# Performance work log

Measured on AMD Instinct MI355X. Metric: run time of the kernel, lower is better.

## Reference

```python
import jax, jax.numpy as jnp
import numpy as np

B, N, F, H1, H2, NC = 1024, 64, 1024, 256, 128, 128
ALPHA = 0.2   # LeakyReLU slope
BN_EPS = 1e-5


def setup_inputs() -> dict:
    key = jax.random.key(0)
    ks = jax.random.split(key, 20)
    d = {}
    d["x"] = jax.random.normal(ks[0], (B, 1, F), dtype=jnp.float32)
    d["neighbor"] = jax.random.normal(ks[1], (B, N, 1, F), dtype=jnp.float32)
    # GraphAttn layer 1 params
    d["W1"] = jax.random.normal(ks[2], (H1, F), dtype=jnp.float32) / np.sqrt(F)
    d["b1"] = jnp.zeros((H1,), dtype=jnp.float32)
    d["a11"] = jax.random.normal(ks[3], (H1,), dtype=jnp.float32) / np.sqrt(H1)
    d["a12"] = jax.random.normal(ks[4], (H1,), dtype=jnp.float32) / np.sqrt(H1)
    d["g1"] = jnp.ones((), dtype=jnp.float32)   # BatchNorm1d(1) weight (scalar)
    d["be1"] = jnp.zeros((), dtype=jnp.float32)  # BatchNorm1d(1) bias
    # GraphAttn layer 2 params
    d["W2"] = jax.random.normal(ks[5], (H2, H1), dtype=jnp.float32) / np.sqrt(H1)
    d["b2"] = jnp.zeros((H2,), dtype=jnp.float32)
    d["a21"] = jax.random.normal(ks[6], (H2,), dtype=jnp.float32) / np.sqrt(H2)
    d["a22"] = jax.random.normal(ks[7], (H2,), dtype=jnp.float32) / np.sqrt(H2)
    d["g2"] = jnp.ones((), dtype=jnp.float32)
    d["be2"] = jnp.zeros((), dtype=jnp.float32)
    # final classifier
    d["Wl"] = jax.random.normal(ks[8], (NC, H2), dtype=jnp.float32) / np.sqrt(H2)
    d["bl"] = jnp.zeros((NC,), dtype=jnp.float32)
    return d


def _l2norm_c(t):
    # torch nf.normalize default: p=2, dim=1 -> here the singleton channel axis (-2)
    n = jnp.sqrt(jnp.sum(t * t, axis=-2, keepdims=True))
    return t / jnp.maximum(n, 1e-12)


def _gat_layer(x, nb, W, b, a_self, a_nb):
    # x: [B,1,Fin], nb: [B,N,1,Fin]
    xh = jnp.einsum('bcf,hf->bch', x, W) + b        # [B,1,H]
    nbh = jnp.einsum('bncf,hf->bnch', nb, W) + b    # [B,N,1,H]
    # att1(x[i]) + att2(neighbor[i]) -> scores over N (C==1 squeezed)
    s = (jnp.einsum('bch,h->bc', xh, a_self)[:, None, :]
         + jnp.einsum('bnch,h->bnc', nbh, a_nb))[..., 0]   # [B,N]
    A = jax.nn.softmax(jax.nn.leaky_relu(s, ALPHA), axis=1)  # softmax over neighbors
    out = jnp.einsum('bn,bnch->bch', A, nbh)        # [B,1,H]
    return out, nbh


def _bn_relu(t, g, b, axes):
    # BatchNorm1d(1) in training mode: stats over all non-channel dims of the tensor
    m = jnp.mean(t, axis=axes, keepdims=True)
    v = jnp.mean(jnp.square(t - m), axis=axes, keepdims=True)
    return jax.nn.relu(g * (t - m) * jax.lax.rsqrt(v + BN_EPS) + b)


def reference(x, neighbor, W1, b1, a11, a12, g1, be1,
              W2, b2, a21, a22, g2, be2, Wl, bl):
    x = _l2norm_c(x)
    nb = _l2norm_c(neighbor)
    x, nb = _gat_layer(x, nb, W1, b1, a11, a12)
    # acvt1 applied to x [B,1,H1] (stats over B,H) and to each neighbor tensor
    # [N,1,H1] separately (per-sample stats -> axes (1,3) of [B,N,1,H1])
    x = _bn_relu(x, g1, be1, axes=(0, 2))
    nb = _bn_relu(nb, g1, be1, axes=(1, 3))
    x, nb = _gat_layer(x, nb, W2, b2, a21, a22)
    x = _bn_relu(x, g2, be2, axes=(0, 2))
    # Flatten -> Dropout(p=0) -> Linear
    logits = jnp.einsum('bh,ch->bc', x.reshape(x.shape[0], -1), Wl) + bl
    return logits
```

## Files before the change

### kernel.cpp

```cpp
#include <hip/hip_runtime.h>
#include <hip/hip_bf16.h>
#include <stdint.h>

#define B_    1024
#define N_    64
#define F_    1024
#define H1_   256
#define H2_   128
#define NC_   128
#define ALPHA 0.2f
#define BN_EPS 1e-5f

typedef __attribute__((ext_vector_type(4))) float  f32x4;
typedef __attribute__((ext_vector_type(8))) __bf16 bf16x8;
typedef __attribute__((ext_vector_type(4))) __bf16 bf16x4;

__device__ inline float sign_ref(float v) {
    float s = copysignf(1.0f, v);
    return (fabsf(v) >= 1e-12f) ? s : v * 1e12f;
}

__device__ __forceinline__ void gload_lds16(const void* g, void* l) {
    auto gp = reinterpret_cast<const __attribute__((address_space(1))) void*>(
        reinterpret_cast<uintptr_t>(g));
    auto lp = reinterpret_cast<__attribute__((address_space(3))) void*>(
        reinterpret_cast<uintptr_t>(l));
    __builtin_amdgcn_global_load_lds(gp, lp, 16, 0, 0);
}

__device__ inline float blk_reduce(float v, float* buf) {
    #pragma unroll
    for (int o = 32; o > 0; o >>= 1) v += __shfl_xor(v, o, 64);
    __syncthreads();
    const int wave = threadIdx.x >> 6, lane = threadIdx.x & 63;
    if (lane == 0) buf[wave] = v;
    __syncthreads();
    float r = 0.f;
    if (threadIdx.x == 0) {
        const int nw = blockDim.x >> 6;
        for (int i = 0; i < nw; ++i) r += buf[i];
    }
    return r;
}

__global__ __launch_bounds__(256) void k_prep(
    const float* __restrict__ W1, const float* __restrict__ W2,
    const float* __restrict__ b1, const float* __restrict__ a11,
    const float* __restrict__ a12, const float* __restrict__ b2,
    const float* __restrict__ a21, const float* __restrict__ a22,
    __bf16* __restrict__ W1b, __bf16* __restrict__ W2b,
    float* __restrict__ w1a, float* __restrict__ w2a,
    float* __restrict__ w2a22, float* __restrict__ cscal)
{
    __shared__ float rbuf[8];
    const int blk = blockIdx.x, tid = threadIdx.x;
    if (blk < 256) {
        const int i0 = blk * 1024 + tid * 4;
        float4 v = *(const float4*)(W1 + i0);
        bf16x4 p = { (__bf16)v.x, (__bf16)v.y, (__bf16)v.z, (__bf16)v.w };
        *(bf16x4*)(W1b + i0) = p;
    } else if (blk < 288) {
        const int i0 = (blk - 256) * 1024 + tid * 4;
        float4 v = *(const float4*)(W2 + i0);
        bf16x4 p = { (__bf16)v.x, (__bf16)v.y, (__bf16)v.z, (__bf16)v.w };
        *(bf16x4*)(W2b + i0) = p;
    } else if (blk < 292) {
        const int f = (blk - 288) * 256 + tid;
        float s1 = 0.f;
        for (int h = 0; h < H1_; ++h) s1 += W1[h * F_ + f] * a11[h];
        w1a[f] = s1;
    } else if (blk == 292) {
        float s1 = 0.f, s2 = 0.f;
        for (int h = 0; h < H2_; ++h) {
            const float w = W2[h * H1_ + tid];
            s1 += w * a21[h]; s2 += w * a22[h];
        }
        w2a[tid] = s1; w2a22[tid] = s2;
    } else {
        float v1 = b1[tid] * a11[tid];
        float v2 = (tid < H2_) ? b2[tid] * a21[tid] : 0.f;
        float v3 = (tid < H2_) ? b2[tid] * a22[tid] : 0.f;
        float r1 = blk_reduce(v1, rbuf);
        float r2 = blk_reduce(v2, rbuf);
        float r3 = blk_reduce(v3, rbuf);
        if (tid == 0) { cscal[0] = r1; cscal[1] = r2; cscal[2] = r3; }
    }
}

__global__ __launch_bounds__(256, 1) void k_gemm1(
    const float* __restrict__ A, const __bf16* __restrict__ Bw,
    const float* __restrict__ bias, __bf16* __restrict__ C)
{
    constexpr int BM = 128, BN = 256, BK = 64, K = F_;
    constexpr int LDA = BK + 8;
    __shared__ __attribute__((aligned(16))) char smem[BM * LDA * 2 + BN * BK * 2];
    __bf16* As = (__bf16*)smem;
    __bf16* Bs = (__bf16*)(smem + BM * LDA * 2);
    __bf16* Cs = Bs;

    const int tid = threadIdx.x;
    const int wave = tid >> 6, lane = tid & 63;
    const int wm = wave & 1, wn = wave >> 1;
    const int rowin = lane & 15, kq = lane >> 4;
    const size_t m0 = (size_t)blockIdx.x * BM;

    f32x4 acc[4][8] = {};

    const int cqA = tid & 15, r0A = tid >> 4;
    const float* Abase = A + m0 * K + cqA * 4;

    for (int k0 = 0; k0 < K; k0 += BK) {
        #pragma unroll
        for (int it = 0; it < 8; ++it) {
            const int s = it * 256 + tid;
            const int r = s >> 3;
            const int c8 = (s & 7) ^ (r & 7);
            gload_lds16(Bw + (size_t)r * K + k0 + c8 * 8, Bs + s * 8);
        }
        #pragma unroll
        for (int rr = 0; rr < 8; ++rr) {
            const int r = r0A + rr * 16;
            float4 v = *(const float4*)(Abase + (size_t)r * K + k0);
            bf16x4 p = { (__bf16)sign_ref(v.x), (__bf16)sign_ref(v.y),
                         (__bf16)sign_ref(v.z), (__bf16)sign_ref(v.w) };
            *(bf16x4*)&As[r * LDA + cqA * 4] = p;
        }
        __syncthreads();
        #pragma unroll
        for (int ks = 0; ks < 2; ++ks) {
            bf16x8 af[4], bv[8];
            #pragma unroll
            for (int mi = 0; mi < 4; ++mi)
                af[mi] = *(const bf16x8*)&As[(wm * 64 + mi * 16 + rowin) * LDA + ks * 32 + kq * 8];
            #pragma unroll
            for (int ni = 0; ni < 8; ++ni) {
                const int r = wn * 128 + ni * 16 + rowin;
                const int c = (ks * 4 + kq) ^ (r & 7);
                bv[ni] = *(const bf16x8*)&Bs[(r * 8 + c) * 8];
            }
            #pragma unroll
            for (int mi = 0; mi < 4; ++mi)
                #pragma unroll
                for (int ni = 0; ni < 8; ++ni)
                    acc[mi][ni] = __builtin_amdgcn_mfma_f32_16x16x32_bf16(
                        af[mi], bv[ni], acc[mi][ni], 0, 0, 0);
        }
        __syncthreads();
    }
    const int cr0 = (lane >> 4) * 4, cc = lane & 15;
    for (int half = 0; half < 2; ++half) {
        if (wm == half) {
            #pragma unroll
            for (int ni = 0; ni < 8; ++ni) {
                const int col = wn * 128 + ni * 16 + cc;
                const float bs = bias[col];
                #pragma unroll
                for (int mi = 0; mi < 4; ++mi)
                    #pragma unroll
                    for (int i = 0; i < 4; ++i)
                        Cs[(mi * 16 + cr0 + i) * 256 + col] =
                            (__bf16)(acc[mi][ni][i] + bs);
            }
        }
        __syncthreads();
        #pragma unroll
        for (int it = 0; it < 8; ++it) {
            const int s = it * 256 + tid;
            const size_t row = m0 + half * 64 + (s >> 5);
            *(bf16x8*)(C + row * 256 + (s & 31) * 8) = *(const bf16x8*)&Cs[s * 8];
        }
        __syncthreads();
    }
}

__global__ __launch_bounds__(256) void k_front(
    const float* __restrict__ x, const float* __restrict__ w1a,
    const __bf16* __restrict__ nbh1, const float* __restrict__ a12,
    const float* __restrict__ g1p, const float* __restrict__ be1p,
    const float* __restrict__ cscal,
    float* __restrict__ out1, float* __restrict__ alpha1,
    float* __restrict__ beta1, float* __restrict__ psum1,
    float* __restrict__ psq1)
{
    __shared__ __attribute__((aligned(16))) __bf16 tile[N_ * H1_];
    __shared__ float a12s[H1_];
    __shared__ float sv[N_];
    __shared__ float rbuf[8];
    __shared__ float sscal[1];

    const int b = blockIdx.x, tid = threadIdx.x;

    const float* xb = x + (size_t)b * F_;
    float xv[4], wa[4];
    #pragma unroll
    for (int i = 0; i < 4; ++i) { xv[i] = xb[tid + i * 256]; wa[i] = w1a[tid + i * 256]; }
    const __bf16* src = nbh1 + (size_t)b * N_ * H1_;
    #pragma unroll
    for (int it = 0; it < 8; ++it)
        gload_lds16(src + (it * 256 + tid) * 8, tile + (it * 256 + tid) * 8);
    a12s[tid] = a12[tid];
    float p0 = 0.f;
    #pragma unroll
    for (int i = 0; i < 4; ++i) p0 += sign_ref(xv[i]) * wa[i];
    float r0 = blk_reduce(p0, rbuf);
    if (tid == 0) sscal[0] = r0 + cscal[0];
    __syncthreads();

    {
        const int n = tid >> 2, q = tid & 3;
        float p = 0.f;
        for (int i = 0; i < 64; ++i) {
            const int h = q * 64 + ((i + tid) & 63);
            p += (float)tile[n * H1_ + h] * a12s[h];
        }
        p += __shfl_xor(p, 1); p += __shfl_xor(p, 2);
        if (q == 0) { float s = sscal[0] + p; sv[n] = s > 0.f ? s : ALPHA * s; }
    }
    __syncthreads();
    if (tid < 64) {
        float s = sv[tid], m = s;
        #pragma unroll
        for (int o = 1; o < 64; o <<= 1) m = fmaxf(m, __shfl_xor(m, o));
        float e = __expf(s - m), t = e;
        #pragma unroll
        for (int o = 1; o < 64; o <<= 1) t += __shfl_xor(t, o);
        sv[tid] = e / t;
    }
    __syncthreads();

    float o1 = 0.f, ss = 0.f, sq = 0.f;
    for (int n2 = 0; n2 < N_; ++n2) {
        const float v = (float)tile[n2 * H1_ + tid];
        o1 += sv[n2] * v; ss += v; sq += v * v;
    }
    out1[(size_t)b * H1_ + tid] = o1;
    {
        const float rs = blk_reduce(ss, rbuf);
        const float rq = blk_reduce(sq, rbuf);
        if (tid == 0) {
            const float inv = 1.f / (float)(N_ * H1_);
            const float mean = rs * inv, var = rq * inv - mean * mean;
            const float a = (*g1p) * rsqrtf(var + BN_EPS);
            alpha1[b] = a; beta1[b] = (*be1p) - a * mean;
        }
        const float rsx = blk_reduce(o1, rbuf);
        const float rqx = blk_reduce(o1 * o1, rbuf);
        if (tid == 0) { psum1[b] = rsx; psq1[b] = rqx; }
    }
}

__global__ __launch_bounds__(256) void k_back(
    const __bf16* __restrict__ nbh1, const float* __restrict__ out1,
    const float* __restrict__ alpha1, const float* __restrict__ beta1,
    const float* __restrict__ psum1, const float* __restrict__ psq1,
    const float* __restrict__ g1p, const float* __restrict__ be1p,
    const float* __restrict__ w2a, const float* __restrict__ w2a22,
    const float* __restrict__ cscal, const __bf16* __restrict__ W2b,
    const float* __restrict__ b2,
    float* __restrict__ out2, float* __restrict__ psum2,
    float* __restrict__ psq2)
{
    __shared__ __attribute__((aligned(16))) __bf16 tile[N_ * H1_];
    __shared__ float wv[H1_];
    __shared__ float w2as[H1_];
    __shared__ float sv[N_];
    __shared__ float g2s[H1_ + 8];
    __shared__ float hpart[H2_];
    __shared__ float rbuf[8];
    __shared__ float scal[3];

    const int b = blockIdx.x, tid = threadIdx.x;

    const __bf16* src = nbh1 + (size_t)b * N_ * H1_;
    #pragma unroll
    for (int it = 0; it < 8; ++it)
        gload_lds16(src + (it * 256 + tid) * 8, tile + (it * 256 + tid) * 8);
    wv[tid] = w2a22[tid]; w2as[tid] = w2a[tid];
    const float o1 = out1[(size_t)b * H1_ + tid];
    const float al = alpha1[b], be = beta1[b];

    {
        float s = 0.f, q = 0.f;
        for (int i = tid; i < B_; i += 256) { s += psum1[i]; q += psq1[i]; }
        const float gs = blk_reduce(s, rbuf);
        const float gq = blk_reduce(q, rbuf);
        if (tid == 0) {
            const float n = (float)(B_ * H1_);
            const float mean = gs / n, var = gq / n - mean * mean;
            const float a = (*g1p) * rsqrtf(var + BN_EPS);
            scal[0] = a; scal[1] = (*be1p) - a * mean;
        }
    }
    __syncthreads();

    {
        const float x2 = fmaxf(fmaf(scal[0], o1, scal[1]), 0.f);
        const float r = blk_reduce(x2 * w2as[tid], rbuf);
        if (tid == 0) scal[2] = r + cscal[1];
    }
    __syncthreads();

    {
        const int n = tid >> 2, q = tid & 3;
        float p = 0.f;
        for (int i = 0; i < 64; ++i) {
            const int h = q * 64 + ((i + tid) & 63);
            const float v = (float)tile[n * H1_ + h];
            p += fmaxf(fmaf(al, v, be), 0.f) * wv[h];
        }
        p += __shfl_xor(p, 1); p += __shfl_xor(p, 2);
        if (q == 0) {
            float s = scal[2] + p + cscal[2];
            sv[n] = s > 0.f ? s : ALPHA * s;
        }
    }
    __syncthreads();
    if (tid < 64) {
        float s = sv[tid], m = s;
        #pragma unroll
        for (int o = 1; o < 64; o <<= 1) m = fmaxf(m, __shfl_xor(m, o));
        float e = __expf(s - m), t = e;
        #pragma unroll
        for (int o = 1; o < 64; o <<= 1) t += __shfl_xor(t, o);
        sv[tid] = e / t;
    }
    __syncthreads();

    {
        float g = 0.f;
        for (int n2 = 0; n2 < N_; ++n2) {
            const float v = (float)tile[n2 * H1_ + tid];
            g += sv[n2] * fmaxf(fmaf(al, v, be), 0.f);
        }
        g2s[tid + (tid >> 5)] = g;
    }
    __syncthreads();

    #pragma unroll 4
    for (int j = 0; j < 16; ++j) {
        const int idx = j * 256 + tid;
        const int h = idx >> 5, k8 = idx & 31;
        const bf16x8 w = ((const bf16x8*)W2b)[idx];
        float p = 0.f;
        #pragma unroll
        for (int i = 0; i < 8; ++i) {
            const int k = k8 * 8 + i;
            p += (float)w[i] * g2s[k + (k >> 5)];
        }
        p += __shfl_xor(p, 1); p += __shfl_xor(p, 2); p += __shfl_xor(p, 4);
        p += __shfl_xor(p, 8); p += __shfl_xor(p, 16);
        if ((tid & 31) == 0) hpart[h] = p;
    }
    __syncthreads();
    {
        float o2 = 0.f;
        if (tid < H2_) o2 = hpart[tid] + b2[tid];
        const float rs2 = blk_reduce(o2, rbuf);
        const float rq2 = blk_reduce(o2 * o2, rbuf);
        if (tid < H2_) out2[(size_t)b * H2_ + tid] = o2;
        if (tid == 0) { psum2[b] = rs2; psq2[b] = rq2; }
    }
}

__global__ __launch_bounds__(128) void k_fin(
    const float* __restrict__ out2, const float* __restrict__ psum2,
    const float* __restrict__ psq2, const float* __restrict__ g2p,
    const float* __restrict__ be2p, const float* __restrict__ Wl,
    const float* __restrict__ bl, float* __restrict__ logits)
{
    __shared__ float xr[H2_];
    __shared__ float Ws[NC_][H2_ + 1];
    __shared__ float axbx[2];
    __shared__ float rbuf[8];
    const int b = blockIdx.x, tid = threadIdx.x;
    {
        float s = 0.f, q = 0.f;
        for (int i = tid; i < B_; i += 128) { s += psum2[i]; q += psq2[i]; }
        const float gs = blk_reduce(s, rbuf);
        const float gq = blk_reduce(q, rbuf);
        if (tid == 0) {
            const float n = (float)(B_ * H2_);
            const float mean = gs / n, var = gq / n - mean * mean;
            const float a = (*g2p) * rsqrtf(var + BN_EPS);
            axbx[0] = a; axbx[1] = (*be2p) - a * mean;
        }
    }
    for (int i = tid; i < NC_ * H2_ / 4; i += 128) {
        float4 v = ((const float4*)Wl)[i];
        const int r = i >> 5, c = (i & 31) * 4;
        Ws[r][c] = v.x; Ws[r][c + 1] = v.y; Ws[r][c + 2] = v.z; Ws[r][c + 3] = v.w;
    }
    __syncthreads();
    xr[tid] = fmaxf(fmaf(axbx[0], out2[(size_t)b * H2_ + tid], axbx[1]), 0.f);
    __syncthreads();
    float acc = bl[tid];
    #pragma unroll 4
    for (int h = 0; h < H2_; ++h) acc += xr[h] * Ws[tid][h];
    logits[(size_t)b * NC_ + tid] = acc;
}

extern "C" void kernel_launch(void* const* d_in, const int* in_sizes, int n_in,
                              void* d_out, int out_size, void* d_ws, size_t ws_size,
                              hipStream_t stream)
{
    const float* x   = (const float*)d_in[0];
    const float* nb  = (const float*)d_in[1];
    const float* W1  = (const float*)d_in[2];
    const float* b1  = (const float*)d_in[3];
    const float* a11 = (const float*)d_in[4];
    const float* a12 = (const float*)d_in[5];
    const float* g1  = (const float*)d_in[6];
    const float* be1 = (const float*)d_in[7];
    const float* W2  = (const float*)d_in[8];
    const float* b2  = (const float*)d_in[9];
    const float* a21 = (const float*)d_in[10];
    const float* a22 = (const float*)d_in[11];
    const float* g2  = (const float*)d_in[12];
    const float* be2 = (const float*)d_in[13];
    const float* Wl  = (const float*)d_in[14];
    const float* bl  = (const float*)d_in[15];
    float* logits = (float*)d_out;

    size_t off = 0;
    auto alc = [&](size_t bytes) {
        void* p = (char*)d_ws + off;
        off = (off + bytes + 255) & ~(size_t)255;
        return p;
    };
    __bf16* W1b   = (__bf16*)alc((size_t)H1_ * F_ * 2);
    __bf16* W2b   = (__bf16*)alc((size_t)H2_ * H1_ * 2);
    float* w1a    = (float*)alc(F_ * 4);
    float* w2a    = (float*)alc(H1_ * 4);
    float* w2a22  = (float*)alc(H1_ * 4);
    float* cscal  = (float*)alc(3 * 4);
    float* sself1 = (float*)alc(B_ * 4);
    float* alpha1 = (float*)alc(B_ * 4);
    float* beta1  = (float*)alc(B_ * 4);
    float* psum1  = (float*)alc(B_ * 4);
    float* psq1   = (float*)alc(B_ * 4);
    float* psum2  = (float*)alc(B_ * 4);
    float* psq2   = (float*)alc(B_ * 4);
    float* out1   = (float*)alc((size_t)B_ * H1_ * 4);
    float* out2   = (float*)alc((size_t)B_ * H2_ * 4);
    __bf16* nbh1  = (__bf16*)alc((size_t)B_ * N_ * H1_ * 2);
    (void)sself1;

    k_prep<<<294, 256, 0, stream>>>(W1, W2, b1, a11, a12, b2, a21, a22,
                                    W1b, W2b, w1a, w2a, w2a22, cscal);
    k_gemm1<<<(B_ * N_) / 128, 256, 0, stream>>>(nb, W1b, b1, nbh1);
    k_front<<<B_, 256, 0, stream>>>(x, w1a, nbh1, a12, g1, be1, cscal,
                                    out1, alpha1, beta1, psum1, psq1);
    k_back<<<B_, 256, 0, stream>>>(nbh1, out1, alpha1, beta1, psum1, psq1,
                                   g1, be1, w2a, w2a22, cscal, W2b, b2,
                                   out2, psum2, psq2);
    k_fin<<<B_, 128, 0, stream>>>(out2, psum2, psq2, g2, be2, Wl, bl, logits);
}
```

Before: 491.0 us.

## Fuse layer-1 attention epilogue into GEMM1 and precompute layer-2 neighbor scores

The separate k_front kernel is folded into the GEMM1 epilogue. Each 128-row GEMM tile covers two samples, so it computes attention scores, softmax, the aggregated output and the BatchNorm statistics directly from the bf16 tile held in LDS. It also computes the layer-2 neighbor attention partial scores and writes them to a new spart buffer, which lets k_back drop its per-neighbor dot-product pass. This removes one kernel launch and a full re-read of nbh1 from global memory. In exchange, the GEMM kernel's tail grows longer and needs more shared memory, and two unroll pragmas are added to the prep loops.

Result: slower. 515.6 us (+5.0%).

```diff
diff --git a/kernel.cpp b/kernel.cpp
--- a/kernel.cpp
+++ b/kernel.cpp
@@ -67,10 +67,12 @@
     } else if (blk < 292) {
         const int f = (blk - 288) * 256 + tid;
         float s1 = 0.f;
+        #pragma unroll 8
         for (int h = 0; h < H1_; ++h) s1 += W1[h * F_ + f] * a11[h];
         w1a[f] = s1;
     } else if (blk == 292) {
         float s1 = 0.f, s2 = 0.f;
+        #pragma unroll 8
         for (int h = 0; h < H2_; ++h) {
             const float w = W2[h * H1_ + tid];
             s1 += w * a21[h]; s2 += w * a22[h];
@@ -89,7 +91,14 @@
 
 __global__ __launch_bounds__(256, 1) void k_gemm1(
     const float* __restrict__ A, const __bf16* __restrict__ Bw,
-    const float* __restrict__ bias, __bf16* __restrict__ C)
+    const float* __restrict__ bias, __bf16* __restrict__ C,
+    const float* __restrict__ x, const float* __restrict__ w1a,
+    const float* __restrict__ a12, const float* __restrict__ w2a22,
+    const float* __restrict__ cscal, const float* __restrict__ g1p,
+    const float* __restrict__ be1p,
+    float* __restrict__ out1, float* __restrict__ alpha1,
+    float* __restrict__ beta1, float* __restrict__ psum1,
+    float* __restrict__ psq1, float* __restrict__ spart)
 {
     constexpr int BM = 128, BN = 256, BK = 64, K = F_;
     constexpr int LDA = BK + 8;
@@ -97,12 +106,36 @@
     __bf16* As = (__bf16*)smem;
     __bf16* Bs = (__bf16*)(smem + BM * LDA * 2);
     __bf16* Cs = Bs;
+    __shared__ float a12s[H1_];
+    __shared__ float w2a22s[H1_];
+    __shared__ float sv[N_];
+    __shared__ float rbuf[8];
+    __shared__ float fscal[4];
 
     const int tid = threadIdx.x;
     const int wave = tid >> 6, lane = tid & 63;
     const int wm = wave & 1, wn = wave >> 1;
     const int rowin = lane & 15, kq = lane >> 4;
     const size_t m0 = (size_t)blockIdx.x * BM;
+    const size_t b0 = (size_t)blockIdx.x * 2;
+
+    {
+        const float* xb = x + b0 * F_;
+        float p0 = 0.f, p1 = 0.f;
+        #pragma unroll
+        for (int i = 0; i < 4; ++i) {
+            const float wa = w1a[tid + i * 256];
+            p0 += sign_ref(xb[tid + i * 256]) * wa;
+            p1 += sign_ref(xb[F_ + tid + i * 256]) * wa;
+        }
+        a12s[tid] = a12[tid]; w2a22s[tid] = w2a22[tid];
+        float r0 = blk_reduce(p0, rbuf);
+        float r1 = blk_reduce(p1, rbuf);
+        if (tid == 0) {
+            const float c1 = cscal[0];
+            fscal[0] = r0 + c1; fscal[1] = r1 + c1;
+        }
+    }
 
     f32x4 acc[4][8] = {};
 
@@ -170,82 +203,64 @@
             *(bf16x8*)(C + row * 256 + (s & 31) * 8) = *(const bf16x8*)&Cs[s * 8];
         }
         __syncthreads();
-    }
-}
-
-__global__ __launch_bounds__(256) void k_front(
-    const float* __restrict__ x, const float* __restrict__ w1a,
-    const __bf16* __restrict__ nbh1, const float* __restrict__ a12,
-    const float* __restrict__ g1p, const float* __restrict__ be1p,
-    const float* __restrict__ cscal,
-    float* __restrict__ out1, float* __restrict__ alpha1,
-    float* __restrict__ beta1, float* __restrict__ psum1,
-    float* __restrict__ psq1)
-{
-    __shared__ __attribute__((aligned(16))) __bf16 tile[N_ * H1_];
-    __shared__ float a12s[H1_];
-    __shared__ float sv[N_];
-    __shared__ float rbuf[8];
-    __shared__ float sscal[1];
-
-    const int b = blockIdx.x, tid = threadIdx.x;
-
-    const float* xb = x + (size_t)b * F_;
-    float xv[4], wa[4];
-    #pragma unroll
-    for (int i = 0; i < 4; ++i) { xv[i] = xb[tid + i * 256]; wa[i] = w1a[tid + i * 256]; }
-    const __bf16* src = nbh1 + (size_t)b * N_ * H1_;
-    #pragma unroll
-    for (int it = 0; it < 8; ++it)
-        gload_lds16(src + (it * 256 + tid) * 8, tile + (it * 256 + tid) * 8);
-    a12s[tid] = a12[tid];
-    float p0 = 0.f;
-    #pragma unroll
-    for (int i = 0; i < 4; ++i) p0 += sign_ref(xv[i]) * wa[i];
-    float r0 = blk_reduce(p0, rbuf);
-    if (tid == 0) sscal[0] = r0 + cscal[0];
-    __syncthreads();
-
-    {
-        const int n = tid >> 2, q = tid & 3;
-        float p = 0.f;
-        for (int i = 0; i < 64; ++i) {
-            const int h = q * 64 + ((i + tid) & 63);
-            p += (float)tile[n * H1_ + h] * a12s[h];
-        }
-        p += __shfl_xor(p, 1); p += __shfl_xor(p, 2);
-        if (q == 0) { float s = sscal[0] + p; sv[n] = s > 0.f ? s : ALPHA * s; }
-    }
-    __syncthreads();
-    if (tid < 64) {
-        float s = sv[tid], m = s;
-        #pragma unroll
-        for (int o = 1; o < 64; o <<= 1) m = fmaxf(m, __shfl_xor(m, o));
-        float e = __expf(s - m), t = e;
-        #pragma unroll
-        for (int o = 1; o < 64; o <<= 1) t += __shfl_xor(t, o);
-        sv[tid] = e / t;
-    }
-    __syncthreads();
-
-    float o1 = 0.f, ss = 0.f, sq = 0.f;
-    for (int n2 = 0; n2 < N_; ++n2) {
-        const float v = (float)tile[n2 * H1_ + tid];
-        o1 += sv[n2] * v; ss += v; sq += v * v;
-    }
-    out1[(size_t)b * H1_ + tid] = o1;
-    {
-        const float rs = blk_reduce(ss, rbuf);
-        const float rq = blk_reduce(sq, rbuf);
-        if (tid == 0) {
-            const float inv = 1.f / (float)(N_ * H1_);
-            const float mean = rs * inv, var = rq * inv - mean * mean;
-            const float a = (*g1p) * rsqrtf(var + BN_EPS);
-            alpha1[b] = a; beta1[b] = (*be1p) - a * mean;
-        }
-        const float rsx = blk_reduce(o1, rbuf);
-        const float rqx = blk_reduce(o1 * o1, rbuf);
-        if (tid == 0) { psum1[b] = rsx; psq1[b] = rqx; }
+
+        const size_t b = b0 + half;
+        {
+            const int n = tid >> 2, q = tid & 3;
+            float p = 0.f;
+            for (int i = 0; i < 64; ++i) {
+                const int h = q * 64 + ((i + tid) & 63);
+                p += (float)Cs[n * 256 + h] * a12s[h];
+            }
+            p += __shfl_xor(p, 1); p += __shfl_xor(p, 2);
+            if (q == 0) { float s = fscal[half] + p; sv[n] = s > 0.f ? s : ALPHA * s; }
+        }
+        __syncthreads();
+        if (tid < 64) {
+            float s = sv[tid], m = s;
+            #pragma unroll
+            for (int o = 1; o < 64; o <<= 1) m = fmaxf(m, __shfl_xor(m, o));
+            float e = __expf(s - m), t = e;
+            #pragma unroll
+            for (int o = 1; o < 64; o <<= 1) t += __shfl_xor(t, o);
+            sv[tid] = e / t;
+        }
+        __syncthreads();
+        float o1 = 0.f, ss = 0.f, sq = 0.f;
+        for (int n2 = 0; n2 < N_; ++n2) {
+            const float v = (float)Cs[n2 * 256 + tid];
+            o1 += sv[n2] * v; ss += v; sq += v * v;
+        }
+        out1[b * H1_ + tid] = o1;
+        {
+            const float rs = blk_reduce(ss, rbuf);
+            const float rq = blk_reduce(sq, rbuf);
+            if (tid == 0) {
+                const float inv = 1.f / (float)(N_ * H1_);
+                const float mean = rs * inv, var = rq * inv - mean * mean;
+                const float a = (*g1p) * rsqrtf(var + BN_EPS);
+                const float bb = (*be1p) - a * mean;
+                alpha1[b] = a; beta1[b] = bb;
+                fscal[2] = a; fscal[3] = bb;
+            }
+            const float rsx = blk_reduce(o1, rbuf);
+            const float rqx = blk_reduce(o1 * o1, rbuf);
+            if (tid == 0) { psum1[b] = rsx; psq1[b] = rqx; }
+        }
+        __syncthreads();
+        {
+            const float al_ = fscal[2], be_ = fscal[3];
+            const int n = tid >> 2, q = tid & 3;
+            float p = 0.f;
+            for (int i = 0; i < 64; ++i) {
+                const int h = q * 64 + ((i + tid) & 63);
+                const float v = (float)Cs[n * 256 + h];
+                p += fmaxf(fmaf(al_, v, be_), 0.f) * w2a22s[h];
+            }
+            p += __shfl_xor(p, 1); p += __shfl_xor(p, 2);
+            if (q == 0) spart[b * N_ + n] = p;
+        }
+        __syncthreads();
     }
 }
 
@@ -254,14 +269,13 @@
     const float* __restrict__ alpha1, const float* __restrict__ beta1,
     const float* __restrict__ psum1, const float* __restrict__ psq1,
     const float* __restrict__ g1p, const float* __restrict__ be1p,
-    const float* __restrict__ w2a, const float* __restrict__ w2a22,
+    const float* __restrict__ w2a, const float* __restrict__ spart,
     const float* __restrict__ cscal, const __bf16* __restrict__ W2b,
     const float* __restrict__ b2,
     float* __restrict__ out2, float* __restrict__ psum2,
     float* __restrict__ psq2)
 {
     __shared__ __attribute__((aligned(16))) __bf16 tile[N_ * H1_];
-    __shared__ float wv[H1_];
     __shared__ float w2as[H1_];
     __shared__ float sv[N_];
     __shared__ float g2s[H1_ + 8];
@@ -275,7 +289,7 @@
     #pragma unroll
     for (int it = 0; it < 8; ++it)
         gload_lds16(src + (it * 256 + tid) * 8, tile + (it * 256 + tid) * 8);
-    wv[tid] = w2a22[tid]; w2as[tid] = w2a[tid];
+    w2as[tid] = w2a[tid];
     const float o1 = out1[(size_t)b * H1_ + tid];
     const float al = alpha1[b], be = beta1[b];
 
@@ -296,27 +310,14 @@
     {
         const float x2 = fmaxf(fmaf(scal[0], o1, scal[1]), 0.f);
         const float r = blk_reduce(x2 * w2as[tid], rbuf);
-        if (tid == 0) scal[2] = r + cscal[1];
-    }
-    __syncthreads();
-
-    {
-        const int n = tid >> 2, q = tid & 3;
-        float p = 0.f;
-        for (int i = 0; i < 64; ++i) {
-            const int h = q * 64 + ((i + tid) & 63);
-            const float v = (float)tile[n * H1_ + h];
-            p += fmaxf(fmaf(al, v, be), 0.f) * wv[h];
-        }
-        p += __shfl_xor(p, 1); p += __shfl_xor(p, 2);
-        if (q == 0) {
-            float s = scal[2] + p + cscal[2];
-            sv[n] = s > 0.f ? s : ALPHA * s;
-        }
-    }
-    __syncthreads();
+        if (tid == 0) scal[2] = r + cscal[1] + cscal[2];
+    }
+    __syncthreads();
+
     if (tid < 64) {
-        float s = sv[tid], m = s;
+        float s = scal[2] + spart[(size_t)b * N_ + tid];
+        s = s > 0.f ? s : ALPHA * s;
+        float m = s;
         #pragma unroll
         for (int o = 1; o < 64; o <<= 1) m = fmaxf(m, __shfl_xor(m, o));
         float e = __expf(s - m), t = e;
@@ -433,25 +434,24 @@
     float* w2a    = (float*)alc(H1_ * 4);
     float* w2a22  = (float*)alc(H1_ * 4);
     float* cscal  = (float*)alc(3 * 4);
-    float* sself1 = (float*)alc(B_ * 4);
     float* alpha1 = (float*)alc(B_ * 4);
     float* beta1  = (float*)alc(B_ * 4);
     float* psum1  = (float*)alc(B_ * 4);
     float* psq1   = (float*)alc(B_ * 4);
     float* psum2  = (float*)alc(B_ * 4);
     float* psq2   = (float*)alc(B_ * 4);
+    float* spart  = (float*)alc((size_t)B_ * N_ * 4);
     float* out1   = (float*)alc((size_t)B_ * H1_ * 4);
     float* out2   = (float*)alc((size_t)B_ * H2_ * 4);
     __bf16* nbh1  = (__bf16*)alc((size_t)B_ * N_ * H1_ * 2);
-    (void)sself1;
 
     k_prep<<<294, 256, 0, stream>>>(W1, W2, b1, a11, a12, b2, a21, a22,
                                     W1b, W2b, w1a, w2a, w2a22, cscal);
-    k_gemm1<<<(B_ * N_) / 128, 256, 0, stream>>>(nb, W1b, b1, nbh1);
-    k_front<<<B_, 256, 0, stream>>>(x, w1a, nbh1, a12, g1, be1, cscal,
-                                    out1, alpha1, beta1, psum1, psq1);
+    k_gemm1<<<(B_ * N_) / 128, 256, 0, stream>>>(
+        nb, W1b, b1, nbh1, x, w1a, a12, w2a22, cscal, g1, be1,
+        out1, alpha1, beta1, psum1, psq1, spart);
     k_back<<<B_, 256, 0, stream>>>(nbh1, out1, alpha1, beta1, psum1, psq1,
-                                   g1, be1, w2a, w2a22, cscal, W2b, b2,
+                                   g1, be1, w2a, spart, cscal, W2b, b2,
                                    out2, psum2, psq2);
     k_fin<<<B_, 128, 0, stream>>>(out2, psum2, psq2, g2, be2, Wl, bl, logits);
 }
```
